# Kernel optimization log

Measured on AMD Instinct MI355X. Metric: run time of the kernel, lower is better.

## Reference

```python
import jax, jax.numpy as jnp
import numpy as np

CHEBYSHEV_K = 5  # number of Chebyshev polynomial terms


def setup_inputs() -> dict:
    key = jax.random.key(0)
    k1, k2, k3 = jax.random.split(key, 3)
    B, N, F_in, F_out = 1024, 512, 16, 8
    x = jax.random.normal(k1, (B, N, F_in), dtype=jnp.float32)
    # symmetric scaled-Laplacian-like matrix, scaled small so recurrence stays stable
    A = jax.random.normal(k2, (N, N), dtype=jnp.float32) / jnp.sqrt(jnp.float32(N))
    L = 0.5 * (A + A.T)
    # xavier-uniform-like weights [K, F_in, F_out]
    limit = np.sqrt(6.0 / (F_in + F_out)).astype(np.float32)
    W = jax.random.uniform(k3, (CHEBYSHEV_K, F_in, F_out), dtype=jnp.float32,
                           minval=-limit, maxval=limit)
    b = jnp.zeros((F_out,), dtype=jnp.float32)
    return {"x": x, "L": L, "W": W, "b": b}


def reference(x, L, W, b):
    # x: [B, N, F_in], L: [N, N], W: [K, F_in, F_out], b: [F_out]
    Lx = lambda z: jnp.einsum('nm,bmf->bnf', L, z)
    Z0 = x
    Z1 = Lx(x)
    out = Z0 @ W[0] + Z1 @ W[1]
    for k in range(2, CHEBYSHEV_K):  # small fixed K, structural loop
        Zk = 2.0 * Lx(Z1) - Z0
        out = out + Zk @ W[k]
        Z0, Z1 = Z1, Zk
    return out + b
```

## Files before the change

kernel.cpp:

```cpp
#include <hip/hip_runtime.h>
#include <cstdint>
#include <cstddef>


typedef __attribute__((ext_vector_type(8))) short  frag_ab;
typedef __attribute__((ext_vector_type(4))) float  frag_cd;

constexpr int BN    = 512;
constexpr int FIN   = 16;
constexpr int FOUT  = 8;
constexpr int BT    = 4;
constexpr int NCOLS = BT * FIN;
constexpr int LDST  = BN + 8;
constexpr int ZBUF  = NCOLS * LDST;

__device__ __forceinline__ uint16_t f2bf(float f) {
    uint32_t u = __builtin_bit_cast(uint32_t, f);
    u += 0x7FFFu + ((u >> 16) & 1u);
    return (uint16_t)(u >> 16);
}
__device__ __forceinline__ float bf2f(uint16_t h) {
    uint32_t u = ((uint32_t)h) << 16;
    return __builtin_bit_cast(float, u);
}

__global__ void cvtL(const float* __restrict__ Lf, uint16_t* __restrict__ Lb) {
    int i = blockIdx.x * 256 + threadIdx.x;
    Lb[i] = f2bf(Lf[i]);
}

__global__ __launch_bounds__(256)
void m2comp(const float* __restrict__ Lf, uint16_t* __restrict__ Mb) {
    const int tid = threadIdx.x;
    const int wv = tid >> 6, lane = tid & 63, lr = lane & 15, q = lane >> 4;
    const int i0 = (blockIdx.x >> 4) * 32 + (wv >> 1) * 16;
    const int j0 = (blockIdx.x & 15) * 32 + (wv & 1) * 16;
    frag_cd acc = {0.f, 0.f, 0.f, 0.f};
    const float* arow = Lf + (size_t)(i0 + lr) * BN;
    const float* brow = Lf + (size_t)(j0 + lr) * BN;
    for (int ks = 0; ks < 16; ++ks) {
        const int kb = ks * 32 + q * 8;
        const float4* ap = reinterpret_cast<const float4*>(arow + kb);
        const float4* bp = reinterpret_cast<const float4*>(brow + kb);
        float4 a0 = ap[0], a1 = ap[1], b0 = bp[0], b1 = bp[1];
        float av[8]  = {a0.x, a0.y, a0.z, a0.w, a1.x, a1.y, a1.z, a1.w};
        float bvv[8] = {b0.x, b0.y, b0.z, b0.w, b1.x, b1.y, b1.z, b1.w};
        frag_ab ah, al, bh, bl;
#pragma unroll
        for (int j = 0; j < 8; ++j) {
            uint16_t h = f2bf(av[j]);
            ah[j] = (short)h;
            al[j] = (short)f2bf(av[j] - bf2f(h));
            uint16_t g = f2bf(bvv[j]);
            bh[j] = (short)g;
            bl[j] = (short)f2bf(bvv[j] - bf2f(g));
        }
        acc = __builtin_amdgcn_mfma_f32_16x16x32_bf16(ah, bh, acc, 0, 0, 0);
        acc = __builtin_amdgcn_mfma_f32_16x16x32_bf16(ah, bl, acc, 0, 0, 0);
        acc = __builtin_amdgcn_mfma_f32_16x16x32_bf16(al, bh, acc, 0, 0, 0);
    }
#pragma unroll
    for (int r = 0; r < 4; ++r) {
        int i = i0 + q * 4 + r, j = j0 + lr;
        float v = 2.f * acc[r] - ((i == j) ? 1.f : 0.f);
        Mb[(size_t)i * BN + j] = f2bf(v);
    }
}

__global__ __launch_bounds__(512, 2)
void cheb2_kernel(const float* __restrict__ x, const uint16_t* __restrict__ Lb,
                  const uint16_t* __restrict__ Mb, const float* __restrict__ W,
                  const float* __restrict__ bvec, float* __restrict__ out) {
    __shared__ uint16_t lds[2 * ZBUF];
    uint16_t* z0 = lds;
    uint16_t* z1 = lds + ZBUF;

    const int tid  = threadIdx.x;
    const int wave = tid >> 6;
    const int lane = tid & 63;
    const int lr   = lane & 15;
    const int q    = lane >> 4;

    const float4* x4 = reinterpret_cast<const float4*>(x + (size_t)blockIdx.x * (BT * BN * FIN));
    for (int s = 0; s < 2; ++s) {
        int a   = tid + s * 512;
        int f0g = a & 3;
        int n8  = (a >> 2) & 63;
        int bl  = a >> 8;
        int jb  = bl * 2048 + n8 * 32 + f0g;
        float4 v[8];
#pragma unroll
        for (int r = 0; r < 8; ++r) v[r] = x4[jb + r * 4];
        int cb = bl * 16 + f0g * 4;
        int nb = n8 * 8;
#pragma unroll
        for (int w = 0; w < 4; ++w) {
            frag_ab pk;
#pragma unroll
            for (int r = 0; r < 8; ++r)
                pk[r] = (short)f2bf(reinterpret_cast<const float*>(&v[r])[w]);
            *reinterpret_cast<frag_ab*>(&z0[(cb + w) * LDST + nb]) = pk;
        }
    }

    frag_ab wf[3];
#pragma unroll
    for (int p = 0; p < 3; ++p) {
        frag_ab t;
#pragma unroll
        for (int jj = 0; jj < 8; ++jj) {
            int k   = q * 8 + jj;
            int ki  = p * 2 + (k >> 4);
            int fin = k & 15;
            float val = 0.0f;
            if (lr < 8) {
                int idx = fin * FOUT + lr;
                if      (ki == 0) val = W[idx] - W[4 * (FIN * FOUT) + idx];
                else if (ki == 1) val = W[1 * (FIN * FOUT) + idx] - W[3 * (FIN * FOUT) + idx];
                else if (ki < 5)  val = W[ki * (FIN * FOUT) + idx];
            }
            t[jj] = (short)f2bf(val);
        }
        wf[p] = t;
    }
    const float bv = (lr < 8) ? bvec[lr] : 0.0f;

    frag_cd accOut[4][4] = {};

    auto loadA = [&](const uint16_t* M, int mt, int ks) -> frag_ab {
        return *reinterpret_cast<const frag_ab*>(M + (size_t)(mt * 16 + lr) * BN + ks * 32 + q * 8);
    };

    frag_cd acc1[4][4];
    frag_cd acc2[4][4];

    auto round = [&](const uint16_t* cur) {
#pragma unroll
        for (int mi = 0; mi < 4; ++mi)
#pragma unroll
            for (int ct = 0; ct < 4; ++ct) {
                acc1[mi][ct] = (frag_cd){0.f, 0.f, 0.f, 0.f};
                acc2[mi][ct] = (frag_cd){0.f, 0.f, 0.f, 0.f};
            }
        for (int ks = 0; ks < 16; ++ks) {
            frag_ab bfr[4];
#pragma unroll
            for (int ct = 0; ct < 4; ++ct)
                bfr[ct] = *reinterpret_cast<const frag_ab*>(
                    cur + (ct * 16 + lr) * LDST + ks * 32 + q * 8);
#pragma unroll
            for (int mi = 0; mi < 4; ++mi) {
                frag_ab a = loadA(Lb, wave + mi * 8, ks);
                frag_ab m = loadA(Mb, wave + mi * 8, ks);
#pragma unroll
                for (int ct = 0; ct < 4; ++ct)
                    acc1[mi][ct] = __builtin_amdgcn_mfma_f32_16x16x32_bf16(
                        a, bfr[ct], acc1[mi][ct], 0, 0, 0);
#pragma unroll
                for (int ct = 0; ct < 4; ++ct)
                    acc2[mi][ct] = __builtin_amdgcn_mfma_f32_16x16x32_bf16(
                        m, bfr[ct], acc2[mi][ct], 0, 0, 0);
            }
        }
    };

    auto wb = [&](frag_cd (&acc)[4][4], uint16_t* dst, float scale) {
#pragma unroll
        for (int mi = 0; mi < 4; ++mi) {
            int row0 = (wave + mi * 8) * 16 + q * 4;
#pragma unroll
            for (int ct = 0; ct < 4; ++ct) {
                uint16_t* dp = dst + (ct * 16 + lr) * LDST + row0;
                ushort4 nv;
                nv.x = f2bf(scale * acc[mi][ct][0]);
                nv.y = f2bf(scale * acc[mi][ct][1]);
                nv.z = f2bf(scale * acc[mi][ct][2]);
                nv.w = f2bf(scale * acc[mi][ct][3]);
                *reinterpret_cast<ushort4*>(dp) = nv;
            }
        }
    };

    auto epi = [&](const uint16_t* bA, const uint16_t* bB, frag_ab wfr) {
        const uint16_t* base = (q < 2) ? bA : bB;
        int finb = (q & 1) * 8;
#pragma unroll
        for (int mi = 0; mi < 4; ++mi) {
            int n = (wave + mi * 8) * 16 + lr;
#pragma unroll
            for (int bt = 0; bt < 4; ++bt) {
                const uint16_t* pp = base + (bt * 16 + finb) * LDST + n;
                frag_ab afr;
#pragma unroll
                for (int jj = 0; jj < 8; ++jj) afr[jj] = (short)pp[jj * LDST];
                accOut[mi][bt] = __builtin_amdgcn_mfma_f32_16x16x32_bf16(
                    afr, wfr, accOut[mi][bt], 0, 0, 0);
            }
        }
    };

    __syncthreads();
    round(z0);
    wb(acc1, z1, 1.f);
    __syncthreads();
    epi(z0, z1, wf[0]);
    __syncthreads();
    wb(acc2, z0, 1.f);
    __syncthreads();
    round(z0);
    wb(acc1, z1, 2.f);
    __syncthreads();
    epi(z0, z1, wf[1]);
    __syncthreads();
    wb(acc2, z0, 2.f);
    __syncthreads();
    epi(z0, z0, wf[2]);

    if (lr < 8) {
        float* ob = out + (size_t)blockIdx.x * BT * BN * FOUT;
#pragma unroll
        for (int mi = 0; mi < 4; ++mi) {
            int row0 = (wave + mi * 8) * 16 + q * 4;
#pragma unroll
            for (int bt = 0; bt < 4; ++bt) {
                float* op = ob + bt * (BN * FOUT) + row0 * FOUT + lr;
                op[0 * FOUT] = accOut[mi][bt][0] + bv;
                op[1 * FOUT] = accOut[mi][bt][1] + bv;
                op[2 * FOUT] = accOut[mi][bt][2] + bv;
                op[3 * FOUT] = accOut[mi][bt][3] + bv;
            }
        }
    }
}

template <bool LBF16>
__global__ __launch_bounds__(512, 2)
void cheb1_kernel(const float* __restrict__ x, const float* __restrict__ Lf,
                  const uint16_t* __restrict__ Lb, const float* __restrict__ W,
                  const float* __restrict__ bvec, float* __restrict__ out) {
    __shared__ uint16_t lds[2 * ZBUF];
    uint16_t* z0 = lds;
    uint16_t* z1 = lds + ZBUF;

    const int tid  = threadIdx.x;
    const int wave = tid >> 6;
    const int lane = tid & 63;
    const int lr   = lane & 15;
    const int q    = lane >> 4;

    const float4* x4 = reinterpret_cast<const float4*>(x + (size_t)blockIdx.x * (BT * BN * FIN));
    for (int s = 0; s < 2; ++s) {
        int a   = tid + s * 512;
        int f0g = a & 3;
        int n8  = (a >> 2) & 63;
        int bl  = a >> 8;
        int jb  = bl * 2048 + n8 * 32 + f0g;
        float4 v[8];
#pragma unroll
        for (int r = 0; r < 8; ++r) v[r] = x4[jb + r * 4];
        int cb = bl * 16 + f0g * 4;
        int nb = n8 * 8;
#pragma unroll
        for (int w = 0; w < 4; ++w) {
            frag_ab pk;
#pragma unroll
            for (int r = 0; r < 8; ++r)
                pk[r] = (short)f2bf(reinterpret_cast<const float*>(&v[r])[w]);
            *reinterpret_cast<frag_ab*>(&z0[(cb + w) * LDST + nb]) = pk;
        }
    }

    frag_ab wf[3];
#pragma unroll
    for (int p = 0; p < 3; ++p) {
        frag_ab t;
#pragma unroll
        for (int jj = 0; jj < 8; ++jj) {
            int k   = q * 8 + jj;
            int ki  = p * 2 + (k >> 4);
            int fin = k & 15;
            float val = (lr < 8 && ki < 5) ? W[ki * (FIN * FOUT) + fin * FOUT + lr] : 0.0f;
            t[jj] = (short)f2bf(val);
        }
        wf[p] = t;
    }
    const float bv = (lr < 8) ? bvec[lr] : 0.0f;

    frag_cd accOut[4][4] = {};

    auto loadA = [&](int mt, int ks) -> frag_ab {
        int row = mt * 16 + lr;
        int kb  = ks * 32 + q * 8;
        if constexpr (LBF16) {
            return *reinterpret_cast<const frag_ab*>(Lb + row * BN + kb);
        } else {
            const float4* p  = reinterpret_cast<const float4*>(Lf + row * BN + kb);
            float4 u0 = p[0], u1 = p[1];
            frag_ab t;
            t[0] = (short)f2bf(u0.x); t[1] = (short)f2bf(u0.y);
            t[2] = (short)f2bf(u0.z); t[3] = (short)f2bf(u0.w);
            t[4] = (short)f2bf(u1.x); t[5] = (short)f2bf(u1.y);
            t[6] = (short)f2bf(u1.z); t[7] = (short)f2bf(u1.w);
            return t;
        }
    };

    auto app = [&](const uint16_t* cur, uint16_t* dst, bool first) {
        frag_cd acc[4][4] = {};
        for (int ks = 0; ks < 16; ++ks) {
            frag_ab bfr[4];
#pragma unroll
            for (int ct = 0; ct < 4; ++ct)
                bfr[ct] = *reinterpret_cast<const frag_ab*>(
                    cur + (ct * 16 + lr) * LDST + ks * 32 + q * 8);
#pragma unroll
            for (int mi = 0; mi < 4; ++mi) {
                frag_ab a = loadA(wave + mi * 8, ks);
#pragma unroll
                for (int ct = 0; ct < 4; ++ct)
                    acc[mi][ct] = __builtin_amdgcn_mfma_f32_16x16x32_bf16(
                        a, bfr[ct], acc[mi][ct], 0, 0, 0);
            }
        }
#pragma unroll
        for (int mi = 0; mi < 4; ++mi) {
            int row0 = (wave + mi * 8) * 16 + q * 4;
#pragma unroll
            for (int ct = 0; ct < 4; ++ct) {
                uint16_t* dp = dst + (ct * 16 + lr) * LDST + row0;
                float pz[4] = {0.f, 0.f, 0.f, 0.f};
                if (!first) {
                    ushort4 pv = *reinterpret_cast<const ushort4*>(dp);
                    pz[0] = bf2f(pv.x); pz[1] = bf2f(pv.y);
                    pz[2] = bf2f(pv.z); pz[3] = bf2f(pv.w);
                }
                ushort4 nv;
                float v0 = acc[mi][ct][0], v1 = acc[mi][ct][1];
                float v2 = acc[mi][ct][2], v3 = acc[mi][ct][3];
                if (!first) {
                    v0 = 2.f * v0 - pz[0]; v1 = 2.f * v1 - pz[1];
                    v2 = 2.f * v2 - pz[2]; v3 = 2.f * v3 - pz[3];
                }
                nv.x = f2bf(v0); nv.y = f2bf(v1); nv.z = f2bf(v2); nv.w = f2bf(v3);
                *reinterpret_cast<ushort4*>(dp) = nv;
            }
        }
    };

    auto epi = [&](const uint16_t* bA, const uint16_t* bB, frag_ab wfr) {
        const uint16_t* base = (q < 2) ? bA : bB;
        int finb = (q & 1) * 8;
#pragma unroll
        for (int mi = 0; mi < 4; ++mi) {
            int n = (wave + mi * 8) * 16 + lr;
#pragma unroll
            for (int bt = 0; bt < 4; ++bt) {
                const uint16_t* pp = base + (bt * 16 + finb) * LDST + n;
                frag_ab afr;
#pragma unroll
                for (int jj = 0; jj < 8; ++jj) afr[jj] = (short)pp[jj * LDST];
                accOut[mi][bt] = __builtin_amdgcn_mfma_f32_16x16x32_bf16(
                    afr, wfr, accOut[mi][bt], 0, 0, 0);
            }
        }
    };

    __syncthreads();
    app(z0, z1, true);
    __syncthreads();
    epi(z0, z1, wf[0]);
    __syncthreads();
    app(z1, z0, false);
    __syncthreads();
    app(z0, z1, false);
    __syncthreads();
    epi(z0, z1, wf[1]);
    __syncthreads();
    app(z1, z0, false);
    __syncthreads();
    epi(z0, z0, wf[2]);

    if (lr < 8) {
        float* ob = out + (size_t)blockIdx.x * BT * BN * FOUT;
#pragma unroll
        for (int mi = 0; mi < 4; ++mi) {
            int row0 = (wave + mi * 8) * 16 + q * 4;
#pragma unroll
            for (int bt = 0; bt < 4; ++bt) {
                float* op = ob + bt * (BN * FOUT) + row0 * FOUT + lr;
                op[0 * FOUT] = accOut[mi][bt][0] + bv;
                op[1 * FOUT] = accOut[mi][bt][1] + bv;
                op[2 * FOUT] = accOut[mi][bt][2] + bv;
                op[3 * FOUT] = accOut[mi][bt][3] + bv;
            }
        }
    }
}

extern "C" void kernel_launch(void* const* d_in, const int* in_sizes, int n_in,
                              void* d_out, int out_size, void* d_ws, size_t ws_size,
                              hipStream_t stream) {
    const float* x  = (const float*)d_in[0];
    const float* Lf = (const float*)d_in[1];
    const float* W  = (const float*)d_in[2];
    const float* bv = (const float*)d_in[3];
    float* out = (float*)d_out;

    const size_t matB = (size_t)BN * BN * sizeof(uint16_t);

    if (ws_size >= 2 * matB) {
        uint16_t* Lb = (uint16_t*)d_ws;
        uint16_t* Mb = Lb + (size_t)BN * BN;
        cvtL<<<dim3(1024), dim3(256), 0, stream>>>(Lf, Lb);
        m2comp<<<dim3(256), dim3(256), 0, stream>>>(Lf, Mb);
        cheb2_kernel<<<dim3(256), dim3(512), 0, stream>>>(x, Lb, Mb, W, bv, out);
    } else if (ws_size >= matB) {
        uint16_t* Lb = (uint16_t*)d_ws;
        cvtL<<<dim3(1024), dim3(256), 0, stream>>>(Lf, Lb);
        cheb1_kernel<true><<<dim3(256), dim3(512), 0, stream>>>(x, Lf, Lb, W, bv, out);
    } else {
        cheb1_kernel<false><<<dim3(256), dim3(512), 0, stream>>>(x, Lf, nullptr, W, bv, out);
    }
}
```

Before: 174.4 us.

## Pre-swizzle L and M into MFMA fragment order and stage output stores via LDS

L and the precomputed M=2L^2-I are now written in MFMA A-fragment order, so each lane's 16-byte A-operand load in the main kernel reads a contiguous chunk per wavefront instead of strided rows. The conversion kernel for L is rewritten to emit this layout with vectorized loads and stores. The final output is staged through LDS and written with coalesced float4 stores rather than scattered 4-byte stores. This adds one extra barrier and requires every producer and consumer of the shared matrices to agree on the swizzle.

```diff
diff --git a/kernel.cpp b/kernel.cpp
--- a/kernel.cpp
+++ b/kernel.cpp
@@ -24,9 +24,31 @@
     return __builtin_bit_cast(float, u);
 }
 
-__global__ void cvtL(const float* __restrict__ Lf, uint16_t* __restrict__ Lb) {
+__device__ __forceinline__ size_t aswz(int row, int k) {
+    return ((size_t)((row >> 4) * 16 + (k >> 5)) * 64
+            + ((k >> 3) & 3) * 16 + (row & 15)) * 8 + (k & 7);
+}
+
+__global__ void cvtL_rm(const float* __restrict__ Lf, uint16_t* __restrict__ Lb) {
     int i = blockIdx.x * 256 + threadIdx.x;
     Lb[i] = f2bf(Lf[i]);
+}
+
+__global__ __launch_bounds__(256)
+void cvtL_swz(const float* __restrict__ Lf, uint16_t* __restrict__ Lb) {
+    int t = blockIdx.x * 256 + threadIdx.x;
+    int f = t >> 6, lane = t & 63;
+    int mt = f >> 4, ks = f & 15;
+    int row = mt * 16 + (lane & 15);
+    int k0  = ks * 32 + (lane >> 4) * 8;
+    const float4* p = reinterpret_cast<const float4*>(Lf + (size_t)row * BN + k0);
+    float4 u0 = p[0], u1 = p[1];
+    frag_ab o;
+    o[0] = (short)f2bf(u0.x); o[1] = (short)f2bf(u0.y);
+    o[2] = (short)f2bf(u0.z); o[3] = (short)f2bf(u0.w);
+    o[4] = (short)f2bf(u1.x); o[5] = (short)f2bf(u1.y);
+    o[6] = (short)f2bf(u1.z); o[7] = (short)f2bf(u1.w);
+    *reinterpret_cast<frag_ab*>(Lb + (size_t)t * 8) = o;
 }
 
 __global__ __launch_bounds__(256)
@@ -63,7 +85,7 @@
     for (int r = 0; r < 4; ++r) {
         int i = i0 + q * 4 + r, j = j0 + lr;
         float v = 2.f * acc[r] - ((i == j) ? 1.f : 0.f);
-        Mb[(size_t)i * BN + j] = f2bf(v);
+        Mb[aswz(i, j)] = f2bf(v);
     }
 }
 
@@ -128,7 +150,8 @@
     frag_cd accOut[4][4] = {};
 
     auto loadA = [&](const uint16_t* M, int mt, int ks) -> frag_ab {
-        return *reinterpret_cast<const frag_ab*>(M + (size_t)(mt * 16 + lr) * BN + ks * 32 + q * 8);
+        return *reinterpret_cast<const frag_ab*>(
+            M + ((size_t)(mt * 16 + ks) * 64 + lane) * 8);
     };
 
     frag_cd acc1[4][4];
@@ -216,20 +239,26 @@
     __syncthreads();
     epi(z0, z0, wf[2]);
 
+    float* fbuf = reinterpret_cast<float*>(z1);
     if (lr < 8) {
-        float* ob = out + (size_t)blockIdx.x * BT * BN * FOUT;
-#pragma unroll
-        for (int mi = 0; mi < 4; ++mi) {
-            int row0 = (wave + mi * 8) * 16 + q * 4;
+#pragma unroll
+        for (int mi = 0; mi < 4; ++mi) {
+            int n0 = (wave + mi * 8) * 16 + q * 4;
 #pragma unroll
             for (int bt = 0; bt < 4; ++bt) {
-                float* op = ob + bt * (BN * FOUT) + row0 * FOUT + lr;
-                op[0 * FOUT] = accOut[mi][bt][0] + bv;
-                op[1 * FOUT] = accOut[mi][bt][1] + bv;
-                op[2 * FOUT] = accOut[mi][bt][2] + bv;
-                op[3 * FOUT] = accOut[mi][bt][3] + bv;
-            }
-        }
+#pragma unroll
+                for (int r = 0; r < 4; ++r)
+                    fbuf[(bt * BN + n0 + r) * FOUT + lr] = accOut[mi][bt][r] + bv;
+            }
+        }
+    }
+    __syncthreads();
+    {
+        const float4* fb4 = reinterpret_cast<const float4*>(fbuf);
+        float4* o4 = reinterpret_cast<float4*>(out + (size_t)blockIdx.x * (BT * BN * FOUT));
+#pragma unroll
+        for (int i = 0; i < 8; ++i)
+            o4[i * 512 + tid] = fb4[i * 512 + tid];
     }
 }
 
@@ -411,12 +440,12 @@
     if (ws_size >= 2 * matB) {
         uint16_t* Lb = (uint16_t*)d_ws;
         uint16_t* Mb = Lb + (size_t)BN * BN;
-        cvtL<<<dim3(1024), dim3(256), 0, stream>>>(Lf, Lb);
+        cvtL_swz<<<dim3(128), dim3(256), 0, stream>>>(Lf, Lb);
         m2comp<<<dim3(256), dim3(256), 0, stream>>>(Lf, Mb);
         cheb2_kernel<<<dim3(256), dim3(512), 0, stream>>>(x, Lb, Mb, W, bv, out);
     } else if (ws_size >= matB) {
         uint16_t* Lb = (uint16_t*)d_ws;
-        cvtL<<<dim3(1024), dim3(256), 0, stream>>>(Lf, Lb);
+        cvtL_rm<<<dim3(1024), dim3(256), 0, stream>>>(Lf, Lb);
         cheb1_kernel<true><<<dim3(256), dim3(512), 0, stream>>>(x, Lf, Lb, W, bv, out);
     } else {
         cheb1_kernel<false><<<dim3(256), dim3(512), 0, stream>>>(x, Lf, nullptr, W, bv, out);
```

New measurement: 146.0 us. 16.3% less time.
